# Kernel optimization log

Measured on AMD Instinct MI355X. Metric: run time of the kernel, lower is better.

The kernel has to match this reference:

```python
import jax, jax.numpy as jnp
import numpy as np

D_MODEL = 768
NUM_HEADS = 12
D_K = D_MODEL // NUM_HEADS
BATCH = 1
SEQ = 4096


def setup_inputs() -> dict:
    key = jax.random.key(0)
    ks = jax.random.split(key, 11)
    s = 0.02
    inp = {
        'Q': jax.random.normal(ks[0], (BATCH, SEQ, D_MODEL), jnp.float32),
        'K': jax.random.normal(ks[1], (BATCH, SEQ, D_MODEL), jnp.float32),
        'V': jax.random.normal(ks[2], (BATCH, SEQ, D_MODEL), jnp.float32),
        'Wq': jax.random.normal(ks[3], (D_MODEL, D_MODEL), jnp.float32) * s,
        'bq': jnp.zeros((D_MODEL,), jnp.float32),
        'Wk': jax.random.normal(ks[4], (D_MODEL, D_MODEL), jnp.float32) * s,
        'bk': jnp.zeros((D_MODEL,), jnp.float32),
        'Wv': jax.random.normal(ks[5], (D_MODEL, D_MODEL), jnp.float32) * s,
        'bv': jnp.zeros((D_MODEL,), jnp.float32),
        'Wo': jax.random.normal(ks[6], (D_MODEL, D_MODEL), jnp.float32) * s,
        'bo': jnp.zeros((D_MODEL,), jnp.float32),
    }
    return inp


def reference(Q, K, V, Wq, bq, Wk, bk, Wv, bv, Wo, bo):
    B, S, _ = Q.shape
    # Linear projections (torch Linear: x @ W^T + b)
    q = Q @ Wq.T + bq
    k = K @ Wk.T + bk
    v = V @ Wv.T + bv
    # split heads: (B, S, D) -> (B, H, S, d_k)
    def split(x):
        return x.reshape(B, S, NUM_HEADS, D_K).transpose(0, 2, 1, 3)
    q, k, v = split(q), split(k), split(v)
    # scaled dot-product attention (dropout = identity in eval)
    scores = jnp.einsum('bhqd,bhkd->bhqk', q, k) / jnp.sqrt(jnp.float32(D_K))
    attn_weights = jax.nn.softmax(scores, axis=-1)
    ctx = jnp.einsum('bhqk,bhkd->bhqd', attn_weights, v)
    # merge heads and output projection
    ctx = ctx.transpose(0, 2, 1, 3).reshape(B, S, D_MODEL)
    output = ctx @ Wo.T + bo
    return (output, attn_weights)
```

## Files before the change

### kernel.cpp

```cpp
#include <hip/hip_runtime.h>
#include <hip/hip_bf16.h>

#define S 4096
#define DM 768
#define NH 12
#define DK 64
#define KSPLIT 2
#define KHALF (S / KSPLIT)
#define RPARTS 8
#define RCHUNK (S / RPARTS)

typedef __bf16 bf16x8 __attribute__((ext_vector_type(8)));
typedef __bf16 bf16x4 __attribute__((ext_vector_type(4)));
typedef float f32x4 __attribute__((ext_vector_type(4)));
using bf16 = __hip_bfloat16;

__device__ inline bf16x8 load_frag(const bf16* p) {
    return *reinterpret_cast<const bf16x8*>(p);
}

__global__ void k_detect(const unsigned int* __restrict__ q, int* __restrict__ flag) {
    const int lane = threadIdx.x;
    int cnt = 0;
    for (int i = lane; i < 1024; i += 64) {
        const unsigned int w = q[i];
        const int e = (w >> 7) & 0xFF;
        if (e >= 192 || (e > 0 && e < 64)) cnt++;
    }
    for (int m = 1; m < 64; m <<= 1) cnt += __shfl_xor(cnt, m, 64);
    if (lane == 0) flag[0] = (cnt > 64) ? 1 : 0;
}

__device__ inline void cast_body(const void* src, bf16* dst, int n, int isf32) {
    const int stride = gridDim.x * 256 * 8;
    for (int i = (blockIdx.x * 256 + threadIdx.x) * 8; i < n; i += stride) {
        if (isf32) {
            const float* s = (const float*)src + i;
            float4 a = *(const float4*)(s);
            float4 b = *(const float4*)(s + 4);
            bf16x8 o;
            o[0] = (__bf16)a.x; o[1] = (__bf16)a.y; o[2] = (__bf16)a.z; o[3] = (__bf16)a.w;
            o[4] = (__bf16)b.x; o[5] = (__bf16)b.y; o[6] = (__bf16)b.z; o[7] = (__bf16)b.w;
            *reinterpret_cast<bf16x8*>(dst + i) = o;
        } else {
            *reinterpret_cast<bf16x8*>(dst + i) =
                *reinterpret_cast<const bf16x8*>((const __bf16*)src + i);
        }
    }
}

__global__ __launch_bounds__(256) void k_cast3(
    const void* s0, const void* s1, const void* s2,
    bf16* d0, bf16* d1, bf16* d2, int n, const int* __restrict__ flag) {
    const int t = blockIdx.y;
    const void* s = (t == 0) ? s0 : (t == 1) ? s1 : s2;
    bf16* d = (t == 0) ? d0 : (t == 1) ? d1 : d2;
    cast_body(s, d, n, flag[0]);
}

__global__ __launch_bounds__(256) void k_cast4(
    const void* s0, const void* s1, const void* s2, const void* s3,
    bf16* d0, bf16* d1, bf16* d2, bf16* d3, int n, const int* __restrict__ flag) {
    const int t = blockIdx.y;
    const void* s = (t == 0) ? s0 : (t == 1) ? s1 : (t == 2) ? s2 : s3;
    bf16* d = (t == 0) ? d0 : (t == 1) ? d1 : (t == 2) ? d2 : d3;
    cast_body(s, d, n, flag[0]);
}

__global__ __launch_bounds__(256) void k_proj(
    const bf16* __restrict__ X, const bf16* __restrict__ W,
    const bf16* __restrict__ bias, void* __restrict__ dstv, int mode,
    const int* __restrict__ flag)
{
    const int isf32 = flag[0];
    const int lane = threadIdx.x & 63;
    const int w    = threadIdx.x >> 6;
    const int lr   = lane & 15, lg = lane >> 4;
    const int rbase = blockIdx.x * 64 + w * 16;
    const int nbase = blockIdx.y * 64;

    f32x4 acc[4] = {};
    const bf16* xrow = X + (size_t)(rbase + lr) * DM + lg * 8;
    for (int kk = 0; kk < DM; kk += 32) {
        bf16x8 a = load_frag(xrow + kk);
#pragma unroll
        for (int nt = 0; nt < 4; ++nt) {
            bf16x8 b = load_frag(W + (size_t)(nbase + nt * 16 + lr) * DM + kk + lg * 8);
            acc[nt] = __builtin_amdgcn_mfma_f32_16x16x32_bf16(a, b, acc[nt], 0, 0, 0);
        }
    }
#pragma unroll
    for (int nt = 0; nt < 4; ++nt) {
        const int col = nbase + nt * 16 + lr;
        const float bv = __bfloat162float(bias[col]);
#pragma unroll
        for (int r = 0; r < 4; ++r) {
            const int row = rbase + lg * 4 + r;
            const float v = acc[nt][r] + bv;
            if (mode == 3) {
                const size_t off = (size_t)row * DM + col;
                if (isf32) ((float*)dstv)[off] = v;
                else       ((bf16*)dstv)[off] = __float2bfloat16(v);
            } else {
                size_t off;
                if (mode == 2) off = (size_t)col * S + row;
                else           off = (size_t)(col >> 6) * (S * DK) + (size_t)row * DK + (col & 63);
                ((bf16*)dstv)[off] = __float2bfloat16(v);
            }
        }
    }
}

__global__ __launch_bounds__(256) void k_rowsum(
    const bf16* __restrict__ qh, const bf16* __restrict__ kh,
    float* __restrict__ rs)
{
    const int lane = threadIdx.x & 63;
    const int w    = threadIdx.x >> 6;
    const int lr   = lane & 15;
    const int lg   = lane >> 4;
    const int h    = blockIdx.y;
    const int part = blockIdx.z;
    const int qw   = blockIdx.x * 256 + w * 64;

    const bf16* qb = qh + (size_t)h * (S * DK);
    const bf16* kb = kh + (size_t)h * (S * DK);
    bf16x8 aq[4][2];
#pragma unroll
    for (int qs = 0; qs < 4; ++qs) {
        aq[qs][0] = load_frag(qb + (size_t)(qw + qs * 16 + lr) * DK + lg * 8);
        aq[qs][1] = load_frag(qb + (size_t)(qw + qs * 16 + lr) * DK + 32 + lg * 8);
    }

    float s[4] = {0.f, 0.f, 0.f, 0.f};
    for (int kp = part * RCHUNK; kp < part * RCHUNK + RCHUNK; kp += 16) {
        bf16x8 b0 = load_frag(kb + (size_t)(kp + lr) * DK + lg * 8);
        bf16x8 b1 = load_frag(kb + (size_t)(kp + lr) * DK + 32 + lg * 8);
#pragma unroll
        for (int qs = 0; qs < 4; ++qs) {
            f32x4 d = {};
            d = __builtin_amdgcn_mfma_f32_16x16x32_bf16(b0, aq[qs][0], d, 0, 0, 0);
            d = __builtin_amdgcn_mfma_f32_16x16x32_bf16(b1, aq[qs][1], d, 0, 0, 0);
            s[qs] += __expf(d[0] * 0.125f) + __expf(d[1] * 0.125f) +
                     __expf(d[2] * 0.125f) + __expf(d[3] * 0.125f);
        }
    }
#pragma unroll
    for (int qs = 0; qs < 4; ++qs) {
        float v = s[qs];
        v += __shfl_xor(v, 16, 64);
        v += __shfl_xor(v, 32, 64);
        if (lg == 0)
            rs[((size_t)part * NH + h) * S + qw + qs * 16 + lr] = v;
    }
}

__global__ __launch_bounds__(256) void k_attn(
    const bf16* __restrict__ qh, const bf16* __restrict__ kh,
    const bf16* __restrict__ vt, const float* __restrict__ rs,
    void* __restrict__ doutv, bf16* __restrict__ ctxp,
    const int* __restrict__ flag)
{
    __shared__ __align__(16) bf16 Plds[4][2][16][136];
    const int isf32 = flag[0];
    const int lane = threadIdx.x & 63;
    const int w    = threadIdx.x >> 6;
    const int lr   = lane & 15, lg = lane >> 4;
    const int h    = blockIdx.y;
    const int half = blockIdx.z;
    const int q0w  = blockIdx.x * 128 + w * 32;
    const int k0   = half * KHALF;

    const bf16* qb = qh + (size_t)h * (S * DK);
    const bf16* kb = kh + (size_t)h * (S * DK);
    const bf16* vb = vt + (size_t)h * (S * DK);

    bf16x8 aq[2][2];
    float  inv[2];
#pragma unroll
    for (int qs = 0; qs < 2; ++qs) {
        const int qr = q0w + qs * 16 + lr;
        aq[qs][0] = load_frag(qb + (size_t)qr * DK + lg * 8);
        aq[qs][1] = load_frag(qb + (size_t)qr * DK + 32 + lg * 8);
        float ssum = 0.f;
#pragma unroll
        for (int p = 0; p < RPARTS; ++p)
            ssum += rs[((size_t)p * NH + h) * S + qr];
        inv[qs] = 1.0f / ssum;
    }

    float* poutF = (float*)doutv + (size_t)S * DM + (size_t)h * S * S;
    bf16*  poutB = (bf16*)doutv  + (size_t)S * DM + (size_t)h * S * S;

    const int fr2 = lane >> 5;
    const int fc2 = (lane & 31) * 4;

    f32x4 acc[2][4] = {};
    for (int tp = 0; tp < KHALF / 128; ++tp) {
#pragma unroll
        for (int tt = 0; tt < 2; ++tt) {
            const int kt = k0 + tp * 128 + tt * 64;
            const int cb = tt * 64;
            bf16x8 vv[4][2];
#pragma unroll
            for (int dt = 0; dt < 4; ++dt) {
                vv[dt][0] = load_frag(vb + (size_t)(dt * 16 + lr) * S + kt + lg * 8);
                vv[dt][1] = load_frag(vb + (size_t)(dt * 16 + lr) * S + kt + 32 + lg * 8);
            }
#pragma unroll
            for (int sub = 0; sub < 4; ++sub) {
                const int kp = kt + sub * 16;
                bf16x8 b0 = load_frag(kb + (size_t)(kp + lr) * DK + lg * 8);
                bf16x8 b1 = load_frag(kb + (size_t)(kp + lr) * DK + 32 + lg * 8);
#pragma unroll
                for (int qs = 0; qs < 2; ++qs) {
                    f32x4 d = {};
                    d = __builtin_amdgcn_mfma_f32_16x16x32_bf16(b0, aq[qs][0], d, 0, 0, 0);
                    d = __builtin_amdgcn_mfma_f32_16x16x32_bf16(b1, aq[qs][1], d, 0, 0, 0);
                    bf16x4 pv;
                    pv[0] = (__bf16)(__expf(d[0] * 0.125f) * inv[qs]);
                    pv[1] = (__bf16)(__expf(d[1] * 0.125f) * inv[qs]);
                    pv[2] = (__bf16)(__expf(d[2] * 0.125f) * inv[qs]);
                    pv[3] = (__bf16)(__expf(d[3] * 0.125f) * inv[qs]);
                    *reinterpret_cast<bf16x4*>(
                        &Plds[w][qs][lr][cb + sub * 16 + 4 * lg]) = pv;
                }
            }
            bf16x8 ap[2][2];
#pragma unroll
            for (int qs = 0; qs < 2; ++qs) {
                ap[qs][0] = *reinterpret_cast<const bf16x8*>(&Plds[w][qs][lr][cb + lg * 8]);
                ap[qs][1] = *reinterpret_cast<const bf16x8*>(&Plds[w][qs][lr][cb + 32 + lg * 8]);
            }
#pragma unroll
            for (int dt = 0; dt < 4; ++dt) {
#pragma unroll
                for (int qs = 0; qs < 2; ++qs) {
                    acc[qs][dt] = __builtin_amdgcn_mfma_f32_16x16x32_bf16(ap[qs][0], vv[dt][0], acc[qs][dt], 0, 0, 0);
                    acc[qs][dt] = __builtin_amdgcn_mfma_f32_16x16x32_bf16(ap[qs][1], vv[dt][1], acc[qs][dt], 0, 0, 0);
                }
            }
        }
        const int ktbase = k0 + tp * 128;
        if (isf32) {
#pragma unroll
            for (int j = 0; j < 16; ++j) {
                const int row = 2 * j + fr2;
                const int qs = row >> 4, rr = row & 15;
                bf16x4 x = *reinterpret_cast<const bf16x4*>(&Plds[w][qs][rr][fc2]);
                f32x4 o;
                o[0] = (float)x[0]; o[1] = (float)x[1];
                o[2] = (float)x[2]; o[3] = (float)x[3];
                __builtin_nontemporal_store(
                    o, reinterpret_cast<f32x4*>(
                           poutF + (size_t)(q0w + row) * S + ktbase + fc2));
            }
        } else {
#pragma unroll
            for (int j = 0; j < 16; ++j) {
                const int row = 2 * j + fr2;
                const int qs = row >> 4, rr = row & 15;
                bf16x4 x = *reinterpret_cast<const bf16x4*>(&Plds[w][qs][rr][fc2]);
                *reinterpret_cast<bf16x4*>(
                    poutB + (size_t)(q0w + row) * S + ktbase + fc2) = x;
            }
        }
    }
    bf16* cp = ctxp + (size_t)half * S * DM;
#pragma unroll
    for (int qs = 0; qs < 2; ++qs)
#pragma unroll
        for (int dt = 0; dt < 4; ++dt)
#pragma unroll
            for (int r = 0; r < 4; ++r)
                cp[(size_t)(q0w + qs * 16 + 4 * lg + r) * DM + h * DK + dt * 16 + lr] =
                    __float2bfloat16(acc[qs][dt][r]);
}

__global__ __launch_bounds__(256) void k_reduce(const bf16* __restrict__ ctxp,
                                               bf16* __restrict__ ctx) {
    const int i = (blockIdx.x * 256 + threadIdx.x) * 8;
    bf16x8 a = *reinterpret_cast<const bf16x8*>(ctxp + i);
    bf16x8 b = *reinterpret_cast<const bf16x8*>(ctxp + (size_t)S * DM + i);
    bf16x8 o;
#pragma unroll
    for (int j = 0; j < 8; ++j) o[j] = (__bf16)((float)a[j] + (float)b[j]);
    *reinterpret_cast<bf16x8*>(ctx + i) = o;
}

extern "C" void kernel_launch(void* const* d_in, const int* in_sizes, int n_in,
                              void* d_out, int out_size, void* d_ws, size_t ws_size,
                              hipStream_t stream) {
    char* wsb = (char*)d_ws;
    int*   flag = (int*)wsb;
    float* rs   = (float*)(wsb + 16);
    bf16*  conv = (bf16*)(wsb + 16 + (size_t)RPARTS * NH * S * 4);

    const size_t nQ = (size_t)S * DM, nW = (size_t)DM * DM, nB = DM;
    bf16* Qc  = conv;
    bf16* Kc  = Qc + nQ;
    bf16* Vc  = Kc + nQ;
    bf16* Wqc = Vc + nQ;
    bf16* Wkc = Wqc + nW;
    bf16* Wvc = Wkc + nW;
    bf16* Woc = Wvc + nW;
    bf16* bqc = Woc + nW;
    bf16* bkc = bqc + nB;
    bf16* bvc = bkc + nB;
    bf16* boc = bvc + nB;
    bf16* qh  = boc + nB;
    bf16* kh  = qh + nQ;
    bf16* vt  = kh + nQ;
    bf16* ctxp = Qc;
    bf16* ctx  = Vc;

    const size_t need = (size_t)((char*)(vt + nQ) - wsb);
    if (ws_size < need) return;

    dim3 blk(256);
    k_detect<<<1, 64, 0, stream>>>((const unsigned int*)d_in[0], flag);

    k_cast3<<<dim3((int)(nQ / 2048), 3), blk, 0, stream>>>(
        d_in[0], d_in[1], d_in[2], Qc, Kc, Vc, (int)nQ, flag);
    k_cast4<<<dim3((int)(nW / 2048), 4), blk, 0, stream>>>(
        d_in[3], d_in[5], d_in[7], d_in[9], Wqc, Wkc, Wvc, Woc, (int)nW, flag);
    k_cast4<<<dim3(1, 4), blk, 0, stream>>>(
        d_in[4], d_in[6], d_in[8], d_in[10], bqc, bkc, bvc, boc, (int)nB, flag);

    k_proj<<<dim3(S / 64, DM / 64), blk, 0, stream>>>(Qc, Wqc, bqc, qh, 0, flag);
    k_proj<<<dim3(S / 64, DM / 64), blk, 0, stream>>>(Kc, Wkc, bkc, kh, 1, flag);
    k_proj<<<dim3(S / 64, DM / 64), blk, 0, stream>>>(Vc, Wvc, bvc, vt, 2, flag);
    k_rowsum<<<dim3(S / 256, NH, RPARTS), blk, 0, stream>>>(qh, kh, rs);
    k_attn<<<dim3(S / 128, NH, KSPLIT), blk, 0, stream>>>(qh, kh, vt, rs, d_out, ctxp, flag);
    k_reduce<<<dim3((int)(nQ / 8 / 256)), blk, 0, stream>>>(ctxp, ctx);
    k_proj<<<dim3(S / 64, DM / 64), blk, 0, stream>>>(ctx, Woc, boc, d_out, 3, flag);
}
```

Baseline: 469.4 us.

## Split attention keys four ways with atomic fp32 context accumulation, fuse QKV launches

Raises the key-dimension split of the attention kernel from 2 to 4, doubling the number of blocks. Each split now adds its partial context into one zeroed fp32 buffer with atomicAdd, instead of writing separate bf16 partial buffers that a reduce kernel then sums. The reduce kernel now only converts fp32 to bf16. The three Q/K/V projections become one launch indexed by blockIdx.z. The cost is an extra zeroing kernel and contention from atomic adds, in exchange for better work balance on the bandwidth-heavy attention-weights write and fewer launches.

```diff
diff --git a/kernel.cpp b/kernel.cpp
--- a/kernel.cpp
+++ b/kernel.cpp
@@ -5,7 +5,7 @@
 #define DM 768
 #define NH 12
 #define DK 64
-#define KSPLIT 2
+#define KSPLIT 4
 #define KHALF (S / KSPLIT)
 #define RPARTS 8
 #define RCHUNK (S / RPARTS)
@@ -67,12 +67,10 @@
     cast_body(s, d, n, flag[0]);
 }
 
-__global__ __launch_bounds__(256) void k_proj(
+__device__ inline void proj_body(
     const bf16* __restrict__ X, const bf16* __restrict__ W,
-    const bf16* __restrict__ bias, void* __restrict__ dstv, int mode,
-    const int* __restrict__ flag)
-{
-    const int isf32 = flag[0];
+    const bf16* __restrict__ bias, void* __restrict__ dstv, int mode, int isf32)
+{
     const int lane = threadIdx.x & 63;
     const int w    = threadIdx.x >> 6;
     const int lr   = lane & 15, lg = lane >> 4;
@@ -111,6 +109,29 @@
     }
 }
 
+__global__ __launch_bounds__(256) void k_proj_qkv(
+    const bf16* __restrict__ Qc, const bf16* __restrict__ Kc, const bf16* __restrict__ Vc,
+    const bf16* __restrict__ Wq, const bf16* __restrict__ Wk, const bf16* __restrict__ Wv,
+    const bf16* __restrict__ bq, const bf16* __restrict__ bk, const bf16* __restrict__ bv,
+    bf16* __restrict__ qh, bf16* __restrict__ kh, bf16* __restrict__ vt,
+    const int* __restrict__ flag)
+{
+    const int z = blockIdx.z;
+    const bf16* X = (z == 0) ? Qc : (z == 1) ? Kc : Vc;
+    const bf16* W = (z == 0) ? Wq : (z == 1) ? Wk : Wv;
+    const bf16* B = (z == 0) ? bq : (z == 1) ? bk : bv;
+    bf16* D      = (z == 0) ? qh : (z == 1) ? kh : vt;
+    proj_body(X, W, B, D, (z == 2) ? 2 : 0, flag[0]);
+}
+
+__global__ __launch_bounds__(256) void k_proj_out(
+    const bf16* __restrict__ X, const bf16* __restrict__ W,
+    const bf16* __restrict__ bias, void* __restrict__ dstv,
+    const int* __restrict__ flag)
+{
+    proj_body(X, W, bias, dstv, 3, flag[0]);
+}
+
 __global__ __launch_bounds__(256) void k_rowsum(
     const bf16* __restrict__ qh, const bf16* __restrict__ kh,
     float* __restrict__ rs)
@@ -158,7 +179,7 @@
 __global__ __launch_bounds__(256) void k_attn(
     const bf16* __restrict__ qh, const bf16* __restrict__ kh,
     const bf16* __restrict__ vt, const float* __restrict__ rs,
-    void* __restrict__ doutv, bf16* __restrict__ ctxp,
+    void* __restrict__ doutv, float* __restrict__ ctxF,
     const int* __restrict__ flag)
 {
     __shared__ __align__(16) bf16 Plds[4][2][16][136];
@@ -266,25 +287,32 @@
             }
         }
     }
-    bf16* cp = ctxp + (size_t)half * S * DM;
 #pragma unroll
     for (int qs = 0; qs < 2; ++qs)
 #pragma unroll
         for (int dt = 0; dt < 4; ++dt)
 #pragma unroll
             for (int r = 0; r < 4; ++r)
-                cp[(size_t)(q0w + qs * 16 + 4 * lg + r) * DM + h * DK + dt * 16 + lr] =
-                    __float2bfloat16(acc[qs][dt][r]);
-}
-
-__global__ __launch_bounds__(256) void k_reduce(const bf16* __restrict__ ctxp,
+                atomicAdd(&ctxF[(size_t)(q0w + qs * 16 + 4 * lg + r) * DM +
+                                h * DK + dt * 16 + lr], acc[qs][dt][r]);
+}
+
+__global__ __launch_bounds__(256) void k_zero(float* __restrict__ p) {
+    const int i = (blockIdx.x * 256 + threadIdx.x) * 4;
+    f32x4 z = {};
+    *reinterpret_cast<f32x4*>(p + i) = z;
+}
+
+__global__ __launch_bounds__(256) void k_reduce(const float* __restrict__ ctxF,
                                                bf16* __restrict__ ctx) {
     const int i = (blockIdx.x * 256 + threadIdx.x) * 8;
-    bf16x8 a = *reinterpret_cast<const bf16x8*>(ctxp + i);
-    bf16x8 b = *reinterpret_cast<const bf16x8*>(ctxp + (size_t)S * DM + i);
+    f32x4 a = *reinterpret_cast<const f32x4*>(ctxF + i);
+    f32x4 b = *reinterpret_cast<const f32x4*>(ctxF + i + 4);
     bf16x8 o;
 #pragma unroll
-    for (int j = 0; j < 8; ++j) o[j] = (__bf16)((float)a[j] + (float)b[j]);
+    for (int j = 0; j < 4; ++j) o[j] = (__bf16)a[j];
+#pragma unroll
+    for (int j = 0; j < 4; ++j) o[4 + j] = (__bf16)b[j];
     *reinterpret_cast<bf16x8*>(ctx + i) = o;
 }
 
@@ -311,8 +339,8 @@
     bf16* qh  = boc + nB;
     bf16* kh  = qh + nQ;
     bf16* vt  = kh + nQ;
-    bf16* ctxp = Qc;
-    bf16* ctx  = Vc;
+    float* ctxF = (float*)Qc;
+    bf16*  ctx  = Vc;
 
     const size_t need = (size_t)((char*)(vt + nQ) - wsb);
     if (ws_size < need) return;
@@ -327,11 +355,11 @@
     k_cast4<<<dim3(1, 4), blk, 0, stream>>>(
         d_in[4], d_in[6], d_in[8], d_in[10], bqc, bkc, bvc, boc, (int)nB, flag);
 
-    k_proj<<<dim3(S / 64, DM / 64), blk, 0, stream>>>(Qc, Wqc, bqc, qh, 0, flag);
-    k_proj<<<dim3(S / 64, DM / 64), blk, 0, stream>>>(Kc, Wkc, bkc, kh, 1, flag);
-    k_proj<<<dim3(S / 64, DM / 64), blk, 0, stream>>>(Vc, Wvc, bvc, vt, 2, flag);
+    k_proj_qkv<<<dim3(S / 64, DM / 64, 3), blk, 0, stream>>>(
+        Qc, Kc, Vc, Wqc, Wkc, Wvc, bqc, bkc, bvc, qh, kh, vt, flag);
+    k_zero<<<dim3((int)(nQ / 1024)), blk, 0, stream>>>(ctxF);
     k_rowsum<<<dim3(S / 256, NH, RPARTS), blk, 0, stream>>>(qh, kh, rs);
-    k_attn<<<dim3(S / 128, NH, KSPLIT), blk, 0, stream>>>(qh, kh, vt, rs, d_out, ctxp, flag);
-    k_reduce<<<dim3((int)(nQ / 8 / 256)), blk, 0, stream>>>(ctxp, ctx);
-    k_proj<<<dim3(S / 64, DM / 64), blk, 0, stream>>>(ctx, Woc, boc, d_out, 3, flag);
-}
+    k_attn<<<dim3(S / 128, NH, KSPLIT), blk, 0, stream>>>(qh, kh, vt, rs, d_out, ctxF, flag);
+    k_reduce<<<dim3((int)(nQ / 2048)), blk, 0, stream>>>(ctxF, ctx);
+    k_proj_out<<<dim3(S / 64, DM / 64), blk, 0, stream>>>(ctx, Woc, boc, d_out, flag);
+}
```

Result: slower. 494.5 us (+5.4%).
